# Optimization experiments

Measured on AMD Instinct MI355X. Metric: run time of the kernel, lower is better.

The kernel has to match this reference:

```python
import jax, jax.numpy as jnp
import numpy as np

N_NODES = 50000
N_EDGES = 800000
D_IN = 256
DIM_H = 256
N_GRAPHS = 500
N_OUT = 10
BN_EPS = 1e-5


def _mlp(h, W1, b1, gamma, beta, mean, var, W2, b2):
    # Linear -> BatchNorm1d (eval, running stats) -> ReLU -> Linear -> ReLU
    h = h @ W1 + b1
    h = (h - mean) * (gamma / jnp.sqrt(var + BN_EPS)) + beta
    h = jax.nn.relu(h)
    return jax.nn.relu(h @ W2 + b2)


def _gin_conv(x, src, dst, params):
    # PyG GINConv with eps=0: out = nn(x + sum_{j in N(i)} x_j)
    agg = jax.ops.segment_sum(x[src], dst, num_segments=N_NODES)
    return _mlp(x + agg, *params)


def setup_inputs() -> dict:
    key = jax.random.key(0)
    ks = jax.random.split(key, 24)
    x = jax.random.normal(ks[0], (N_NODES, D_IN), dtype=jnp.float32)
    edge_index = jax.random.randint(ks[1], (2, N_EDGES), 0, N_NODES, dtype=jnp.int64)
    batch = jnp.sort(jax.random.randint(ks[2], (N_NODES,), 0, N_GRAPHS, dtype=jnp.int64))

    def lin(k, fan_in, fan_out):
        s = 1.0 / np.sqrt(fan_in)
        kw, kb = jax.random.split(k)
        W = jax.random.uniform(kw, (fan_in, fan_out), minval=-s, maxval=s, dtype=jnp.float32)
        b = jax.random.uniform(kb, (fan_out,), minval=-s, maxval=s, dtype=jnp.float32)
        return W, b

    def bn(k, d):
        k1, k2, k3, k4 = jax.random.split(k, 4)
        gamma = 1.0 + 0.1 * jax.random.normal(k1, (d,), dtype=jnp.float32)
        beta = 0.1 * jax.random.normal(k2, (d,), dtype=jnp.float32)
        mean = 0.1 * jax.random.normal(k3, (d,), dtype=jnp.float32)
        var = jax.random.uniform(k4, (d,), minval=0.5, maxval=1.5, dtype=jnp.float32)
        return gamma, beta, mean, var

    W1a, b1a = lin(ks[3], D_IN, DIM_H)
    g1a, be1a, m1a, v1a = bn(ks[4], DIM_H)
    W2a, b2a = lin(ks[5], DIM_H, DIM_H)
    W1b, b1b = lin(ks[6], DIM_H, DIM_H)
    g1b, be1b, m1b, v1b = bn(ks[7], DIM_H)
    W2b, b2b = lin(ks[8], DIM_H, DIM_H)
    lin1_W, lin1_b = lin(ks[9], DIM_H * 2, DIM_H * 3)
    lin2_W, lin2_b = lin(ks[10], DIM_H * 3, N_OUT)

    return dict(x=x, edge_index=edge_index, batch=batch,
                W1a=W1a, b1a=b1a, g1a=g1a, be1a=be1a, m1a=m1a, v1a=v1a, W2a=W2a, b2a=b2a,
                W1b=W1b, b1b=b1b, g1b=g1b, be1b=be1b, m1b=m1b, v1b=v1b, W2b=W2b, b2b=b2b,
                lin1_W=lin1_W, lin1_b=lin1_b, lin2_W=lin2_W, lin2_b=lin2_b)


def reference(x, edge_index, batch,
              W1a, b1a, g1a, be1a, m1a, v1a, W2a, b2a,
              W1b, b1b, g1b, be1b, m1b, v1b, W2b, b2b,
              lin1_W, lin1_b, lin2_W, lin2_b):
    src, dst = edge_index[0], edge_index[1]
    h1 = _gin_conv(x, src, dst, (W1a, b1a, g1a, be1a, m1a, v1a, W2a, b2a))
    h2 = _gin_conv(h1, src, dst, (W1b, b1b, g1b, be1b, m1b, v1b, W2b, b2b))
    p1 = jax.ops.segment_sum(h1, batch, num_segments=N_GRAPHS)  # global_add_pool
    p2 = jax.ops.segment_sum(h2, batch, num_segments=N_GRAPHS)
    h = jnp.concatenate([p1, p2], axis=1)
    h = jax.nn.relu(h @ lin1_W + lin1_b)
    # dropout p=0.6 is identity in eval mode
    h = h @ lin2_W + lin2_b
    return jax.nn.log_softmax(h, axis=1)
```

## Files before the change

kernel.cpp:

```cpp
#include <hip/hip_runtime.h>

#define N_NODES 50000
#define MPAD 50176
#define N_EDGES 800000
#define DIM 256
#define N_GRAPHS 500
#define N_OUT 10
#define BN_EPS 1e-5f
#define SCAN_BS 1024
#define KSPLIT 4
#define SORT_CAP 96

typedef unsigned int u32;
typedef short bf16x8 __attribute__((ext_vector_type(8)));
typedef unsigned short us8 __attribute__((ext_vector_type(8)));
typedef float f32x4 __attribute__((ext_vector_type(4)));

typedef __attribute__((address_space(1))) const unsigned int gas_u32;
typedef __attribute__((address_space(3))) unsigned int las_u32;

__device__ inline void g2l16(const void* g, void* l) {
    __builtin_amdgcn_global_load_lds((gas_u32*)g, (las_u32*)l, 16, 0, 0);
}

__device__ inline float b2f(unsigned short u) {
    union { u32 i; float f; } c; c.i = ((u32)u) << 16; return c.f;
}
__device__ inline unsigned short f2b(float f) {
    u32 x = __builtin_bit_cast(u32, f);
    return (unsigned short)((x + 0x7FFFu + ((x >> 16) & 1u)) >> 16);
}

__device__ inline int mid_addr(int row, int col) {
    return row * 512 + ((((col >> 3) ^ (row & 31)) << 4) | ((col & 7) << 1));
}

__global__ void zero_i(int* __restrict__ p, int n) {
    int i = blockIdx.x * blockDim.x + threadIdx.x;
    if (i < n) p[i] = 0;
}
__global__ void hist_dst(const int* __restrict__ dst, int* __restrict__ deg) {
    int e = blockIdx.x * blockDim.x + threadIdx.x;
    if (e < N_EDGES) atomicAdd(&deg[dst[e]], 1);
}
__global__ void scan_phase1(const int* __restrict__ deg, int* __restrict__ rowptr,
                            int* __restrict__ bsum, int n) {
    __shared__ int sh[SCAN_BS];
    int i = blockIdx.x * SCAN_BS + threadIdx.x;
    int v = (i < n) ? deg[i] : 0;
    sh[threadIdx.x] = v;
    __syncthreads();
    for (int off = 1; off < SCAN_BS; off <<= 1) {
        int t = (threadIdx.x >= off) ? sh[threadIdx.x - off] : 0;
        __syncthreads();
        sh[threadIdx.x] += t;
        __syncthreads();
    }
    if (i < n) rowptr[i] = sh[threadIdx.x] - v;
    if (threadIdx.x == SCAN_BS - 1) bsum[blockIdx.x] = sh[threadIdx.x];
}
__global__ void scan_phase2(int* __restrict__ bsum, int nb) {
    if (threadIdx.x == 0 && blockIdx.x == 0) {
        int run = 0;
        for (int b = 0; b < nb; b++) { int v = bsum[b]; bsum[b] = run; run += v; }
    }
}
__global__ void scan_phase3(int* __restrict__ rowptr, int* __restrict__ cursor,
                            const int* __restrict__ bsum, int n) {
    int i = blockIdx.x * SCAN_BS + threadIdx.x;
    if (i < n) {
        int v = rowptr[i] + bsum[blockIdx.x];
        rowptr[i] = v;
        cursor[i] = v;
    }
    if (i == 0) rowptr[n] = N_EDGES;
}
__global__ void fill_csr(const int* __restrict__ src, const int* __restrict__ dst,
                         int* __restrict__ cursor, int* __restrict__ col) {
    int e = blockIdx.x * blockDim.x + threadIdx.x;
    if (e < N_EDGES) {
        int p = atomicAdd(&cursor[dst[e]], 1);
        col[p] = src[e];
    }
}
__global__ void sort_csr(const int* __restrict__ rowptr, int* __restrict__ col) {
    __shared__ int buf[4][SORT_CAP];
    int node = blockIdx.x * 4 + (threadIdx.x >> 6);
    if (node >= N_NODES) return;
    int lane = threadIdx.x & 63;
    int w = threadIdx.x >> 6;
    int s = rowptr[node], e = rowptr[node + 1];
    int L = e - s;
    if (L <= 1 || L > SORT_CAP) return;
    for (int i = lane; i < L; i += 64) buf[w][i] = col[s + i];
    asm volatile("s_waitcnt lgkmcnt(0) vmcnt(0)" ::: "memory");
    for (int pass = 0; pass < L; pass++) {
        int base = 2 * lane + (pass & 1);
        if (base + 1 < L) {
            int a = buf[w][base], b = buf[w][base + 1];
            if (a > b) { buf[w][base] = b; buf[w][base + 1] = a; }
        }
        asm volatile("s_waitcnt lgkmcnt(0)" ::: "memory");
    }
    for (int i = lane; i < L; i += 64) col[s + i] = buf[w][i];
}
__global__ void graph_starts(const int* __restrict__ batch, int* __restrict__ gstart) {
    int g = blockIdx.x * blockDim.x + threadIdx.x;
    if (g > N_GRAPHS) return;
    if (g == N_GRAPHS) { gstart[g] = N_NODES; return; }
    int lo = 0, hi = N_NODES;
    while (lo < hi) { int mid = (lo + hi) >> 1; if (batch[mid] < g) lo = mid + 1; else hi = mid; }
    gstart[g] = lo;
}

__global__ void conv_x(const float4* __restrict__ in, ushort4* __restrict__ out, int n4) {
    int i = blockIdx.x * blockDim.x + threadIdx.x;
    if (i < n4) {
        float4 v = in[i];
        ushort4 o; o.x = f2b(v.x); o.y = f2b(v.y); o.z = f2b(v.z); o.w = f2b(v.w);
        out[i] = o;
    }
}
__global__ void conv_wt4(const float* __restrict__ W0, const float* __restrict__ W1,
                         const float* __restrict__ W2, const float* __restrict__ W3,
                         unsigned short* __restrict__ Wt) {
    int mat = blockIdx.y;
    const float* W = (mat == 0) ? W0 : (mat == 1) ? W1 : (mat == 2) ? W2 : W3;
    int n = blockIdx.x;
    int k = threadIdx.x;
    Wt[((size_t)mat << 16) + (size_t)n * 256 + k] = f2b(W[(size_t)k * 256 + n]);
}
__global__ void make_ss(const float* __restrict__ bias, const float* __restrict__ gamma,
                        const float* __restrict__ beta, const float* __restrict__ mean,
                        const float* __restrict__ var, float* __restrict__ scale,
                        float* __restrict__ shift) {
    int i = threadIdx.x;
    float s = gamma[i] * rsqrtf(var[i] + BN_EPS);
    scale[i] = s;
    shift[i] = (bias[i] - mean[i]) * s + beta[i];
}

__global__ void gather_bf(const unsigned short* __restrict__ feat,
                          const int* __restrict__ col,
                          const int* __restrict__ rowptr,
                          unsigned short* __restrict__ out) {
    int node = blockIdx.x * 4 + (threadIdx.x >> 6);
    if (node >= N_NODES) return;
    int lane = threadIdx.x & 63;
    int half = lane >> 5;
    int d8 = (lane & 31) * 8;
    float acc[8];
    #pragma unroll
    for (int j = 0; j < 8; j++) acc[j] = 0.f;
    if (half == 0) {
        us8 own = *reinterpret_cast<const us8*>(&feat[(size_t)node * DIM + d8]);
        #pragma unroll
        for (int j = 0; j < 8; j++) acc[j] = b2f((unsigned short)own[j]);
    }
    int s = rowptr[node], e = rowptr[node + 1];
    int i = s + half;
    for (; i + 6 < e; i += 8) {
        int n0 = col[i], n1 = col[i + 2], n2 = col[i + 4], n3 = col[i + 6];
        us8 v0 = *reinterpret_cast<const us8*>(&feat[(size_t)n0 * DIM + d8]);
        us8 v1 = *reinterpret_cast<const us8*>(&feat[(size_t)n1 * DIM + d8]);
        us8 v2 = *reinterpret_cast<const us8*>(&feat[(size_t)n2 * DIM + d8]);
        us8 v3 = *reinterpret_cast<const us8*>(&feat[(size_t)n3 * DIM + d8]);
        #pragma unroll
        for (int j = 0; j < 8; j++)
            acc[j] += (b2f((unsigned short)v0[j]) + b2f((unsigned short)v1[j]))
                    + (b2f((unsigned short)v2[j]) + b2f((unsigned short)v3[j]));
    }
    for (; i < e; i += 2) {
        int n0 = col[i];
        us8 v0 = *reinterpret_cast<const us8*>(&feat[(size_t)n0 * DIM + d8]);
        #pragma unroll
        for (int j = 0; j < 8; j++) acc[j] += b2f((unsigned short)v0[j]);
    }
    #pragma unroll
    for (int j = 0; j < 8; j++) acc[j] += __shfl_xor(acc[j], 32, 64);
    if (half == 0) {
        us8 o;
        #pragma unroll
        for (int j = 0; j < 8; j++) o[j] = (short)f2b(acc[j]);
        *reinterpret_cast<us8*>(&out[(size_t)node * DIM + d8]) = o;
    }
}

__global__ __launch_bounds__(256, 2)
void fused_mlp(const unsigned short* __restrict__ A,
               const unsigned short* __restrict__ W1t,
               const unsigned short* __restrict__ W2t,
               const float* __restrict__ scale1,
               const float* __restrict__ shift1,
               const float* __restrict__ shift2,
               unsigned short* __restrict__ H, int M) {
    __shared__ __align__(16) unsigned short Asb[2][64 * 32];
    __shared__ __align__(16) unsigned short Bsb[2][256 * 32];
    __shared__ __align__(16) unsigned short midb[64 * 256];

    int t = threadIdx.x;
    int wave = t >> 6, lane = t & 63;
    int m0 = blockIdx.x * 64;
    int wc = wave * 64;
    int rsel = lane & 15;
    int ksel = (lane >> 4) * 8;
    int cr = lane >> 4;

    float s1[4], sh1[4], sh2[4];
    #pragma unroll
    for (int n = 0; n < 4; n++) {
        int colg = wc + n * 16 + rsel;
        s1[n]  = scale1[colg];
        sh1[n] = shift1[colg];
        sh2[n] = shift2[colg];
    }

    int cb = (t & 3) * 16;
    const char* Ab  = (const char*)A   + (size_t)(m0 + (t >> 2)) * 512 + cb;
    const char* B1b = (const char*)W1t + (size_t)(t >> 2) * 512 + cb;
    const char* B2b = (const char*)W2t + (size_t)(t >> 2) * 512 + cb;

    f32x4 acc[4][4];
    #pragma unroll
    for (int m = 0; m < 4; m++)
        #pragma unroll
        for (int n = 0; n < 4; n++)
            acc[m][n] = (f32x4){0.f, 0.f, 0.f, 0.f};

    #pragma unroll
    for (int p = 0; p < 2; p++) {
        size_t ko = (size_t)p * 64;
        g2l16(Ab + ko, (char*)Asb[p] + (size_t)t * 16);
        #pragma unroll
        for (int i = 0; i < 4; i++)
            g2l16(B1b + (size_t)i * 32768 + ko, (char*)Bsb[p] + (size_t)(i * 256 + t) * 16);
    }

    #pragma unroll
    for (int ks = 0; ks < 8; ks++) {
        const int cur = ks & 1;
        __syncthreads();

        const unsigned short* As = Asb[cur];
        const unsigned short* Bs = Bsb[cur];
        bf16x8 af[4], bfr[4];
        #pragma unroll
        for (int m = 0; m < 4; m++)
            af[m] = *(const bf16x8*)&As[(size_t)(m * 16 + rsel) * 32 + ksel];
        #pragma unroll
        for (int n = 0; n < 4; n++)
            bfr[n] = *(const bf16x8*)&Bs[(size_t)(wc + n * 16 + rsel) * 32 + ksel];
        #pragma unroll
        for (int m = 0; m < 4; m++)
            #pragma unroll
            for (int n = 0; n < 4; n++)
                acc[m][n] = __builtin_amdgcn_mfma_f32_16x16x32_bf16(af[m], bfr[n], acc[m][n], 0, 0, 0);

        __syncthreads();
        if (ks + 2 < 8) {
            size_t ko = (size_t)(ks + 2) * 64;
            g2l16(Ab + ko, (char*)Asb[cur] + (size_t)t * 16);
            #pragma unroll
            for (int i = 0; i < 4; i++)
                g2l16(B1b + (size_t)i * 32768 + ko, (char*)Bsb[cur] + (size_t)(i * 256 + t) * 16);
        } else if (ks == 6) {
            #pragma unroll
            for (int i = 0; i < 4; i++)
                g2l16(B2b + (size_t)i * 32768, (char*)Bsb[0] + (size_t)(i * 256 + t) * 16);
        } else {
            #pragma unroll
            for (int i = 0; i < 4; i++)
                g2l16(B2b + (size_t)i * 32768 + 64, (char*)Bsb[1] + (size_t)(i * 256 + t) * 16);
        }
    }

    #pragma unroll
    for (int n = 0; n < 4; n++) {
        int colg = wc + n * 16 + rsel;
        #pragma unroll
        for (int m = 0; m < 4; m++) {
            int rowb = m * 16 + cr * 4;
            #pragma unroll
            for (int r = 0; r < 4; r++) {
                float v = fmaxf(acc[m][n][r] * s1[n] + sh1[n], 0.f);
                *(unsigned short*)((char*)midb + mid_addr(rowb + r, colg)) = f2b(v);
                acc[m][n][r] = 0.f;
            }
        }
    }

    #pragma unroll
    for (int ks = 0; ks < 8; ks++) {
        const int cur = ks & 1;
        __syncthreads();

        const unsigned short* Bs = Bsb[cur];
        bf16x8 af[4], bfr[4];
        #pragma unroll
        for (int m = 0; m < 4; m++)
            af[m] = *(const bf16x8*)((const char*)midb + mid_addr(m * 16 + rsel, ks * 32 + ksel));
        #pragma unroll
        for (int n = 0; n < 4; n++)
            bfr[n] = *(const bf16x8*)&Bs[(size_t)(wc + n * 16 + rsel) * 32 + ksel];
        #pragma unroll
        for (int m = 0; m < 4; m++)
            #pragma unroll
            for (int n = 0; n < 4; n++)
                acc[m][n] = __builtin_amdgcn_mfma_f32_16x16x32_bf16(af[m], bfr[n], acc[m][n], 0, 0, 0);

        __syncthreads();
        if (ks + 2 < 8) {
            size_t ko = (size_t)(ks + 2) * 64;
            #pragma unroll
            for (int i = 0; i < 4; i++)
                g2l16(B2b + (size_t)i * 32768 + ko, (char*)Bsb[cur] + (size_t)(i * 256 + t) * 16);
        }
    }

    #pragma unroll
    for (int n = 0; n < 4; n++) {
        int colg = wc + n * 16 + rsel;
        #pragma unroll
        for (int m = 0; m < 4; m++) {
            int rowb = m0 + m * 16 + cr * 4;
            #pragma unroll
            for (int r = 0; r < 4; r++) {
                int row = rowb + r;
                if (row < M) {
                    float v = fmaxf(acc[m][n][r] + sh2[n], 0.f);
                    H[(size_t)row * 256 + colg] = f2b(v);
                }
            }
        }
    }
}

__global__ void pool_seg(const unsigned short* __restrict__ h1,
                         const unsigned short* __restrict__ h2,
                         const int* __restrict__ gstart,
                         float* __restrict__ pcat) {
    __shared__ float red1[8][256];
    __shared__ float red2[8][256];
    int g = blockIdx.x;
    int t = threadIdx.x;
    int sub = t >> 5;
    int d8 = (t & 31) * 8;
    float a1[8], a2[8];
    #pragma unroll
    for (int j = 0; j < 8; j++) { a1[j] = 0.f; a2[j] = 0.f; }
    int s = gstart[g], e = gstart[g + 1];
    for (int n = s + sub; n < e; n += 8) {
        us8 v1 = *reinterpret_cast<const us8*>(&h1[(size_t)n * DIM + d8]);
        us8 v2 = *reinterpret_cast<const us8*>(&h2[(size_t)n * DIM + d8]);
        #pragma unroll
        for (int j = 0; j < 8; j++) {
            a1[j] += b2f((unsigned short)v1[j]);
            a2[j] += b2f((unsigned short)v2[j]);
        }
    }
    #pragma unroll
    for (int j = 0; j < 8; j++) {
        red1[sub][d8 + j] = a1[j];
        red2[sub][d8 + j] = a2[j];
    }
    __syncthreads();
    float o1 = 0.f, o2 = 0.f;
    #pragma unroll
    for (int k = 0; k < 8; k++) { o1 += red1[k][t]; o2 += red2[k][t]; }
    pcat[(size_t)g * 512 + t]       = o1;
    pcat[(size_t)g * 512 + 256 + t] = o2;
}

__global__ void head1(const float* __restrict__ A,
                      const float* __restrict__ W1,
                      float* __restrict__ Hpart) {
    __shared__ float As[16][65];
    __shared__ float Bs[16][65];
    int t = threadIdx.x;
    int m0 = blockIdx.y * 64;
    int n0 = blockIdx.x * 64;
    int kz = blockIdx.z * (512 / KSPLIT);
    int tx = t & 15, ty = t >> 4;
    float acc[4][4] = {};
    for (int k0 = kz; k0 < kz + 512 / KSPLIT; k0 += 16) {
        #pragma unroll
        for (int i = 0; i < 4; i++) {
            int r = (t >> 4) + i * 16;
            int k = t & 15;
            int gr = m0 + r;
            As[k][r] = (gr < N_GRAPHS) ? A[(size_t)gr * 512 + k0 + k] : 0.f;
        }
        #pragma unroll
        for (int i = 0; i < 4; i++) {
            int k = (t >> 6) + i * 4;
            int n = t & 63;
            Bs[k][n] = W1[(size_t)(k0 + k) * 768 + n0 + n];
        }
        __syncthreads();
        #pragma unroll
        for (int k = 0; k < 16; k++) {
            float a[4], b[4];
            #pragma unroll
            for (int i = 0; i < 4; i++) a[i] = As[k][ty * 4 + i];
            #pragma unroll
            for (int j = 0; j < 4; j++) b[j] = Bs[k][tx * 4 + j];
            #pragma unroll
            for (int i = 0; i < 4; i++)
                #pragma unroll
                for (int j = 0; j < 4; j++)
                    acc[i][j] += a[i] * b[j];
        }
        __syncthreads();
    }
    float* Hz = Hpart + (size_t)blockIdx.z * N_GRAPHS * 768;
    #pragma unroll
    for (int i = 0; i < 4; i++) {
        int gm = m0 + ty * 4 + i;
        if (gm >= N_GRAPHS) continue;
        #pragma unroll
        for (int j = 0; j < 4; j++) {
            int gn = n0 + tx * 4 + j;
            Hz[(size_t)gm * 768 + gn] = acc[i][j];
        }
    }
}

__global__ void head2(const float* __restrict__ Hpart, const float* __restrict__ b1,
                      const float* __restrict__ W2, const float* __restrict__ b2,
                      float* __restrict__ out) {
    int g = blockIdx.x;
    int lane = threadIdx.x;
    float part[N_OUT];
    #pragma unroll
    for (int o = 0; o < N_OUT; o++) part[o] = 0.f;
    for (int k = lane; k < 768; k += 64) {
        float hv = b1[k];
        #pragma unroll
        for (int z = 0; z < KSPLIT; z++)
            hv += Hpart[((size_t)z * N_GRAPHS + g) * 768 + k];
        hv = fmaxf(hv, 0.f);
        #pragma unroll
        for (int o = 0; o < N_OUT; o++) part[o] += hv * W2[(size_t)k * N_OUT + o];
    }
    #pragma unroll
    for (int o = 0; o < N_OUT; o++) {
        #pragma unroll
        for (int off = 32; off > 0; off >>= 1)
            part[o] += __shfl_down(part[o], off, 64);
    }
    if (lane == 0) {
        float logits[N_OUT];
        float mx = -1e30f;
        #pragma unroll
        for (int o = 0; o < N_OUT; o++) { logits[o] = part[o] + b2[o]; mx = fmaxf(mx, logits[o]); }
        float ssum = 0.f;
        #pragma unroll
        for (int o = 0; o < N_OUT; o++) ssum += expf(logits[o] - mx);
        float lse = logf(ssum);
        #pragma unroll
        for (int o = 0; o < N_OUT; o++)
            out[(size_t)g * N_OUT + o] = logits[o] - mx - lse;
    }
}

extern "C" void kernel_launch(void* const* d_in, const int* in_sizes, int n_in,
                              void* d_out, int out_size, void* d_ws, size_t ws_size,
                              hipStream_t stream) {
    const float* x     = (const float*)d_in[0];
    const int*   ei    = (const int*)d_in[1];
    const int*   batch = (const int*)d_in[2];
    const float* W1a = (const float*)d_in[3];
    const float* b1a = (const float*)d_in[4];
    const float* g1a = (const float*)d_in[5];
    const float* be1a= (const float*)d_in[6];
    const float* m1a = (const float*)d_in[7];
    const float* v1a = (const float*)d_in[8];
    const float* W2a = (const float*)d_in[9];
    const float* b2a = (const float*)d_in[10];
    const float* W1b = (const float*)d_in[11];
    const float* b1b = (const float*)d_in[12];
    const float* g1b = (const float*)d_in[13];
    const float* be1b= (const float*)d_in[14];
    const float* m1b = (const float*)d_in[15];
    const float* v1b = (const float*)d_in[16];
    const float* W2b = (const float*)d_in[17];
    const float* b2b = (const float*)d_in[18];
    const float* lin1_W = (const float*)d_in[19];
    const float* lin1_b = (const float*)d_in[20];
    const float* lin2_W = (const float*)d_in[21];
    const float* lin2_b = (const float*)d_in[22];

    const size_t NBUF = (size_t)MPAD * DIM;
    char* ws = (char*)d_ws;
    unsigned short* agg  = (unsigned short*)ws;            ws += NBUF * 2;
    unsigned short* h1   = (unsigned short*)ws;            ws += NBUF * 2;
    unsigned short* h2   = (unsigned short*)ws;            ws += NBUF * 2;
    unsigned short* x_bf = (unsigned short*)ws;            ws += (size_t)N_NODES * DIM * 2;
    unsigned short* Wt   = (unsigned short*)ws;            ws += 4 * 65536 * 2;
    float* ss    = (float*)ws;                             ws += 4 * 256 * 4;
    float* pcat  = (float*)ws;                             ws += (size_t)N_GRAPHS * 512 * 4;
    float* Hpart = (float*)ws;                             ws += (size_t)KSPLIT * N_GRAPHS * 768 * 4;
    int* deg     = (int*)ws;                               ws += (size_t)N_NODES * 4;
    int* cursor  = (int*)ws;                               ws += (size_t)N_NODES * 4;
    int* rowptr  = (int*)ws;                               ws += (size_t)(N_NODES + 1) * 4;
    int* bsum    = (int*)ws;                               ws += 64 * 4;
    int* col     = (int*)ws;                               ws += (size_t)N_EDGES * 4;
    int* gstart  = (int*)ws;

    const int* srcE = ei;
    const int* dstE = ei + N_EDGES;

    const int nscan = (N_NODES + SCAN_BS - 1) / SCAN_BS;

    zero_i<<<(N_NODES + 255) / 256, 256, 0, stream>>>(deg, N_NODES);
    hist_dst<<<(N_EDGES + 255) / 256, 256, 0, stream>>>(dstE, deg);
    scan_phase1<<<nscan, SCAN_BS, 0, stream>>>(deg, rowptr, bsum, N_NODES);
    scan_phase2<<<1, 64, 0, stream>>>(bsum, nscan);
    scan_phase3<<<nscan, SCAN_BS, 0, stream>>>(rowptr, cursor, bsum, N_NODES);
    fill_csr<<<(N_EDGES + 255) / 256, 256, 0, stream>>>(srcE, dstE, cursor, col);
    sort_csr<<<(N_NODES + 3) / 4, 256, 0, stream>>>(rowptr, col);
    graph_starts<<<2, 256, 0, stream>>>(batch, gstart);

    conv_x<<<(N_NODES * DIM / 4 + 255) / 256, 256, 0, stream>>>(
        (const float4*)x, (ushort4*)x_bf, N_NODES * DIM / 4);
    dim3 wt_grid(256, 4);
    conv_wt4<<<wt_grid, 256, 0, stream>>>(W1a, W2a, W1b, W2b, Wt);
    make_ss<<<1, 256, 0, stream>>>(b1a, g1a, be1a, m1a, v1a, ss + 0 * 512, ss + 0 * 512 + 256);
    make_ss<<<1, 256, 0, stream>>>(b1b, g1b, be1b, m1b, v1b, ss + 1 * 512, ss + 1 * 512 + 256);

    gather_bf<<<(N_NODES + 3) / 4, 256, 0, stream>>>(x_bf, col, rowptr, agg);
    fused_mlp<<<MPAD / 64, 256, 0, stream>>>(agg, Wt + 0 * 65536, Wt + 1 * 65536,
                                             ss + 0 * 512, ss + 0 * 512 + 256, b2a, h1, N_NODES);

    gather_bf<<<(N_NODES + 3) / 4, 256, 0, stream>>>(h1, col, rowptr, agg);
    fused_mlp<<<MPAD / 64, 256, 0, stream>>>(agg, Wt + 2 * 65536, Wt + 3 * 65536,
                                             ss + 1 * 512, ss + 1 * 512 + 256, b2b, h2, N_NODES);

    pool_seg<<<N_GRAPHS, 256, 0, stream>>>(h1, h2, gstart, pcat);
    dim3 h1grid(12, 8, KSPLIT);
    head1<<<h1grid, 256, 0, stream>>>(pcat, lin1_W, Hpart);
    head2<<<N_GRAPHS, 64, 0, stream>>>(Hpart, lin1_b, lin2_W, lin2_b, (float*)d_out);
}
```

Measured before the change: 364.7 us.

## Use single-buffered 64-wide K tiles with XOR-swizzled LDS layout in fused MLP

Replaces the double-buffered 32-wide K pipeline in fused_mlp with single-buffered 64-wide K tiles whose 16-byte chunks are XOR-swizzled by row, for both GEMMs. The swizzle is meant to remove LDS bank conflicts on the MFMA fragment reads, and the wider tile halves the number of barrier pairs. In exchange it gives up the prefetch overlap: each tile load must finish before compute starts, and the W2 load no longer overlaps the tail of the first GEMM.

```diff
diff --git a/kernel.cpp b/kernel.cpp
--- a/kernel.cpp
+++ b/kernel.cpp
@@ -194,8 +194,8 @@
                const float* __restrict__ shift1,
                const float* __restrict__ shift2,
                unsigned short* __restrict__ H, int M) {
-    __shared__ __align__(16) unsigned short Asb[2][64 * 32];
-    __shared__ __align__(16) unsigned short Bsb[2][256 * 32];
+    __shared__ __align__(16) unsigned short Asb[64 * 64];
+    __shared__ __align__(16) unsigned short Bsb[256 * 64];
     __shared__ __align__(16) unsigned short midb[64 * 256];
 
     int t = threadIdx.x;
@@ -203,7 +203,7 @@
     int m0 = blockIdx.x * 64;
     int wc = wave * 64;
     int rsel = lane & 15;
-    int ksel = (lane >> 4) * 8;
+    int kgrp = lane >> 4;
     int cr = lane >> 4;
 
     float s1[4], sh1[4], sh2[4];
@@ -215,11 +215,6 @@
         sh2[n] = shift2[colg];
     }
 
-    int cb = (t & 3) * 16;
-    const char* Ab  = (const char*)A   + (size_t)(m0 + (t >> 2)) * 512 + cb;
-    const char* B1b = (const char*)W1t + (size_t)(t >> 2) * 512 + cb;
-    const char* B2b = (const char*)W2t + (size_t)(t >> 2) * 512 + cb;
-
     f32x4 acc[4][4];
     #pragma unroll
     for (int m = 0; m < 4; m++)
@@ -227,51 +222,48 @@
         for (int n = 0; n < 4; n++)
             acc[m][n] = (f32x4){0.f, 0.f, 0.f, 0.f};
 
-    #pragma unroll
-    for (int p = 0; p < 2; p++) {
-        size_t ko = (size_t)p * 64;
-        g2l16(Ab + ko, (char*)Asb[p] + (size_t)t * 16);
-        #pragma unroll
-        for (int i = 0; i < 4; i++)
-            g2l16(B1b + (size_t)i * 32768 + ko, (char*)Bsb[p] + (size_t)(i * 256 + t) * 16);
-    }
-
-    #pragma unroll
-    for (int ks = 0; ks < 8; ks++) {
-        const int cur = ks & 1;
-        __syncthreads();
-
-        const unsigned short* As = Asb[cur];
-        const unsigned short* Bs = Bsb[cur];
-        bf16x8 af[4], bfr[4];
-        #pragma unroll
-        for (int m = 0; m < 4; m++)
-            af[m] = *(const bf16x8*)&As[(size_t)(m * 16 + rsel) * 32 + ksel];
-        #pragma unroll
-        for (int n = 0; n < 4; n++)
-            bfr[n] = *(const bf16x8*)&Bs[(size_t)(wc + n * 16 + rsel) * 32 + ksel];
-        #pragma unroll
-        for (int m = 0; m < 4; m++)
-            #pragma unroll
-            for (int n = 0; n < 4; n++)
-                acc[m][n] = __builtin_amdgcn_mfma_f32_16x16x32_bf16(af[m], bfr[n], acc[m][n], 0, 0, 0);
-
-        __syncthreads();
-        if (ks + 2 < 8) {
-            size_t ko = (size_t)(ks + 2) * 64;
-            g2l16(Ab + ko, (char*)Asb[cur] + (size_t)t * 16);
-            #pragma unroll
-            for (int i = 0; i < 4; i++)
-                g2l16(B1b + (size_t)i * 32768 + ko, (char*)Bsb[cur] + (size_t)(i * 256 + t) * 16);
-        } else if (ks == 6) {
-            #pragma unroll
-            for (int i = 0; i < 4; i++)
-                g2l16(B2b + (size_t)i * 32768, (char*)Bsb[0] + (size_t)(i * 256 + t) * 16);
-        } else {
-            #pragma unroll
-            for (int i = 0; i < 4; i++)
-                g2l16(B2b + (size_t)i * 32768 + 64, (char*)Bsb[1] + (size_t)(i * 256 + t) * 16);
-        }
+    int arow0 = t >> 3, achk0 = t & 7;
+    int arow1 = (256 + t) >> 3, achk1 = t & 7;
+    const char* Abase = (const char*)A + (size_t)m0 * 512;
+
+    for (int ks = 0; ks < 4; ks++) {
+        size_t ko = (size_t)ks * 128;
+        g2l16(Abase + (size_t)arow0 * 512 + ko + ((achk0 ^ (arow0 & 7)) << 4),
+              (char*)Asb + (size_t)t * 16);
+        g2l16(Abase + (size_t)arow1 * 512 + ko + ((achk1 ^ (arow1 & 7)) << 4),
+              (char*)Asb + (size_t)(256 + t) * 16);
+        #pragma unroll
+        for (int i = 0; i < 8; i++) {
+            int s = i * 256 + t;
+            int brow = s >> 3, bchk = s & 7;
+            g2l16((const char*)W1t + (size_t)brow * 512 + ko + ((bchk ^ (brow & 7)) << 4),
+                  (char*)Bsb + (size_t)s * 16);
+        }
+        __syncthreads();
+
+        #pragma unroll
+        for (int ksub = 0; ksub < 2; ksub++) {
+            bf16x8 af[4], bfr[4];
+            int kchunk = ksub * 4 + kgrp;
+            #pragma unroll
+            for (int m = 0; m < 4; m++) {
+                int row = m * 16 + rsel;
+                af[m] = *(const bf16x8*)((const char*)Asb + (size_t)row * 128
+                                         + ((kchunk ^ (row & 7)) << 4));
+            }
+            #pragma unroll
+            for (int n = 0; n < 4; n++) {
+                int row = wc + n * 16 + rsel;
+                bfr[n] = *(const bf16x8*)((const char*)Bsb + (size_t)row * 128
+                                          + ((kchunk ^ (row & 7)) << 4));
+            }
+            #pragma unroll
+            for (int m = 0; m < 4; m++)
+                #pragma unroll
+                for (int n = 0; n < 4; n++)
+                    acc[m][n] = __builtin_amdgcn_mfma_f32_16x16x32_bf16(af[m], bfr[n], acc[m][n], 0, 0, 0);
+        }
+        __syncthreads();
     }
 
     #pragma unroll
@@ -289,32 +281,38 @@
         }
     }
 
-    #pragma unroll
-    for (int ks = 0; ks < 8; ks++) {
-        const int cur = ks & 1;
-        __syncthreads();
-
-        const unsigned short* Bs = Bsb[cur];
-        bf16x8 af[4], bfr[4];
-        #pragma unroll
-        for (int m = 0; m < 4; m++)
-            af[m] = *(const bf16x8*)((const char*)midb + mid_addr(m * 16 + rsel, ks * 32 + ksel));
-        #pragma unroll
-        for (int n = 0; n < 4; n++)
-            bfr[n] = *(const bf16x8*)&Bs[(size_t)(wc + n * 16 + rsel) * 32 + ksel];
-        #pragma unroll
-        for (int m = 0; m < 4; m++)
-            #pragma unroll
-            for (int n = 0; n < 4; n++)
-                acc[m][n] = __builtin_amdgcn_mfma_f32_16x16x32_bf16(af[m], bfr[n], acc[m][n], 0, 0, 0);
-
-        __syncthreads();
-        if (ks + 2 < 8) {
-            size_t ko = (size_t)(ks + 2) * 64;
-            #pragma unroll
-            for (int i = 0; i < 4; i++)
-                g2l16(B2b + (size_t)i * 32768 + ko, (char*)Bsb[cur] + (size_t)(i * 256 + t) * 16);
-        }
+    for (int ks = 0; ks < 4; ks++) {
+        size_t ko = (size_t)ks * 128;
+        #pragma unroll
+        for (int i = 0; i < 8; i++) {
+            int s = i * 256 + t;
+            int brow = s >> 3, bchk = s & 7;
+            g2l16((const char*)W2t + (size_t)brow * 512 + ko + ((bchk ^ (brow & 7)) << 4),
+                  (char*)Bsb + (size_t)s * 16);
+        }
+        __syncthreads();
+
+        #pragma unroll
+        for (int ksub = 0; ksub < 2; ksub++) {
+            bf16x8 af[4], bfr[4];
+            int kchunk = ksub * 4 + kgrp;
+            int kcol = ks * 64 + ksub * 32 + kgrp * 8;
+            #pragma unroll
+            for (int m = 0; m < 4; m++)
+                af[m] = *(const bf16x8*)((const char*)midb + mid_addr(m * 16 + rsel, kcol));
+            #pragma unroll
+            for (int n = 0; n < 4; n++) {
+                int row = wc + n * 16 + rsel;
+                bfr[n] = *(const bf16x8*)((const char*)Bsb + (size_t)row * 128
+                                          + ((kchunk ^ (row & 7)) << 4));
+            }
+            #pragma unroll
+            for (int m = 0; m < 4; m++)
+                #pragma unroll
+                for (int n = 0; n < 4; n++)
+                    acc[m][n] = __builtin_amdgcn_mfma_f32_16x16x32_bf16(af[m], bfr[n], acc[m][n], 0, 0, 0);
+        }
+        __syncthreads();
     }
 
     #pragma unroll
```

Measured after the change: 361.4 us. Within noise of the previous version (-0.9%).
